# Performance work log

Measured on AMD Instinct MI355X. Metric: run time of the kernel, lower is better.

Reference implementation:

```python
import jax, jax.numpy as jnp
import numpy as np

S, H, I, E, TOP_K = 8192, 2048, 2048, 8, 2


def setup_inputs() -> dict:
    key = jax.random.key(0)
    k0, k1, k2, k3 = jax.random.split(key, 4)
    scale = 1.0 / np.sqrt(H)
    return {
        "hidden_states": jax.random.normal(k0, (S, H), dtype=jnp.float32),
        "w_gate": jax.random.normal(k1, (E, H), dtype=jnp.float32) * scale,
        "w1": jax.random.normal(k2, (E, 2 * I, H), dtype=jnp.float32) * scale,
        "w2": jax.random.normal(k3, (E, H, I), dtype=jnp.float32) * (1.0 / np.sqrt(I)),
        "top_k": TOP_K,
    }


def reference(hidden_states, w_gate, w1, w2, top_k):
    # Router: logits -> float32 softmax -> top-k -> renormalize
    router_logits = hidden_states @ w_gate.T                      # [S, E]
    probs = jax.nn.softmax(router_logits.astype(jnp.float32), axis=-1)
    top_p, top_i = jax.lax.top_k(probs, top_k)                    # [S, k]
    top_p = top_p / jnp.sum(top_p, axis=-1, keepdims=True)

    n_tok, n_exp = probs.shape
    # Dense combine weights [S, E]; zero for non-selected experts.
    combine = jnp.zeros((n_tok, n_exp), dtype=probs.dtype)
    combine = combine.at[jnp.arange(n_tok)[:, None], top_i].add(top_p)

    inter = w2.shape[2]
    out = jnp.zeros_like(hidden_states)
    # Loop over the small fixed expert set; masked-combine gives exact
    # fused_moe semantics (scatter-combine of weighted expert outputs).
    for e in range(n_exp):
        gu = hidden_states @ w1[e].T                              # [S, 2I]
        gate, up = gu[:, :inter], gu[:, inter:]
        h = jax.nn.silu(gate) * up                                # SiluAndMul
        out = out + combine[:, e:e + 1].astype(hidden_states.dtype) * (h @ w2[e].T)
    return out, router_logits
```

## Files before the change

kernel.cpp:

```cpp
#include <hip/hip_runtime.h>
#include <hip/hip_bf16.h>
#include <stdint.h>

#define S_TOK 8192
#define H_DIM 2048
#define I_DIM 2048
#define E_NUM 8

typedef __attribute__((ext_vector_type(4))) float f32x4;
typedef __attribute__((ext_vector_type(8))) short bf16x8;
typedef __attribute__((ext_vector_type(8))) unsigned short u16x8;

#define MFMA16(a, b, c) __builtin_amdgcn_mfma_f32_16x16x32_bf16((a), (b), (c), 0, 0, 0)

__device__ __forceinline__ unsigned short f2bf(float f) {
    unsigned int u = __float_as_uint(f);
    unsigned int r = (u + 0x7FFFu + ((u >> 16) & 1u)) >> 16;
    return (unsigned short)r;
}
__device__ __forceinline__ float bf2f(unsigned short u) {
    return __uint_as_float((unsigned int)u << 16);
}

__device__ __forceinline__ void cvt8(const float* __restrict__ s, unsigned short* __restrict__ d) {
    float4 v0 = *(const float4*)s;
    float4 v1 = *(const float4*)(s + 4);
    u16x8 o;
    o[0] = f2bf(v0.x); o[1] = f2bf(v0.y); o[2] = f2bf(v0.z); o[3] = f2bf(v0.w);
    o[4] = f2bf(v1.x); o[5] = f2bf(v1.y); o[6] = f2bf(v1.z); o[7] = f2bf(v1.w);
    *(u16x8*)d = o;
}

__device__ __forceinline__ void async_copy16(void* lds, const void* g) {
    __builtin_amdgcn_global_load_lds(
        (const __attribute__((address_space(1))) void*)(uintptr_t)g,
        (__attribute__((address_space(3))) void*)(uintptr_t)lds,
        16, 0, 0);
}

__device__ __forceinline__ int xcd_swizzle(int bid, int nwg) {
    int cpx = nwg >> 3;
    return (bid & 7) * cpx + (bid >> 3);
}

__global__ void cvt_kernel(const float* __restrict__ src, unsigned short* __restrict__ dst, long n) {
    long i0 = ((long)blockIdx.x * blockDim.x + threadIdx.x) * 8;
    long stride = (long)gridDim.x * blockDim.x * 8;
    for (long i = i0; i < n; i += stride) cvt8(src + i, dst + i);
}

template<int HALF>
__device__ __forceinline__ void cvt_w1_half_body(const float* __restrict__ src,
                                                 unsigned short* __restrict__ dst,
                                                 long i0, long stride) {
    const long CH = 1L << 21;
    const long TOT = (long)E_NUM * 2 * CH;
    for (long j = i0; j < TOT; j += stride) {
        long e = j >> 22;
        long piece = (j >> 21) & 1;
        long off = j & (CH - 1);
        long g = (e << 23) + ((piece * 2 + HALF) << 21) + off;
        cvt8(src + g, dst + g);
    }
}

__global__ void router_kernel(const float* __restrict__ hs, const float* __restrict__ wg,
                              float* __restrict__ logits,
                              unsigned int* __restrict__ tchoice, float* __restrict__ twgt,
                              unsigned short* __restrict__ hsb,
                              const float* __restrict__ w1src, unsigned short* __restrict__ w1dst,
                              int cvt_blks) {
    if ((int)blockIdx.x >= S_TOK) {
        long i0 = ((long)((int)blockIdx.x - S_TOK) * blockDim.x + threadIdx.x) * 8;
        long stride = (long)cvt_blks * blockDim.x * 8;
        cvt_w1_half_body<0>(w1src, w1dst, i0, stride);
        return;
    }
    int t = blockIdx.x;
    int tid = threadIdx.x;
    const float* hrow = hs + (size_t)t * H_DIM;
    float4 h0 = *(const float4*)(hrow + tid * 8);
    float4 h1 = *(const float4*)(hrow + tid * 8 + 4);
    u16x8 o;
    o[0] = f2bf(h0.x); o[1] = f2bf(h0.y); o[2] = f2bf(h0.z); o[3] = f2bf(h0.w);
    o[4] = f2bf(h1.x); o[5] = f2bf(h1.y); o[6] = f2bf(h1.z); o[7] = f2bf(h1.w);
    *(u16x8*)(hsb + (size_t)t * H_DIM + tid * 8) = o;

    float p[E_NUM];
#pragma unroll
    for (int e = 0; e < E_NUM; ++e) {
        const float* w = wg + (size_t)e * H_DIM + tid * 8;
        float4 w0 = *(const float4*)(w);
        float4 w1v = *(const float4*)(w + 4);
        p[e] = h0.x * w0.x + h0.y * w0.y + h0.z * w0.z + h0.w * w0.w +
               h1.x * w1v.x + h1.y * w1v.y + h1.z * w1v.z + h1.w * w1v.w;
    }
#pragma unroll
    for (int e = 0; e < E_NUM; ++e)
#pragma unroll
        for (int d = 32; d > 0; d >>= 1) p[e] += __shfl_xor(p[e], d, 64);

    __shared__ float red[4][E_NUM];
    int wave = tid >> 6, lane = tid & 63;
    if (lane == 0) {
#pragma unroll
        for (int e = 0; e < E_NUM; ++e) red[wave][e] = p[e];
    }
    __syncthreads();
    if (tid == 0) {
        float l[E_NUM];
#pragma unroll
        for (int e = 0; e < E_NUM; ++e) l[e] = red[0][e] + red[1][e] + red[2][e] + red[3][e];
#pragma unroll
        for (int e = 0; e < E_NUM; ++e) logits[(size_t)t * E_NUM + e] = l[e];
        int i1 = 0;
#pragma unroll
        for (int e = 1; e < E_NUM; ++e) if (l[e] > l[i1]) i1 = e;
        int i2 = (i1 == 0) ? 1 : 0;
#pragma unroll
        for (int e = 0; e < E_NUM; ++e) if (e != i1 && l[e] > l[i2]) i2 = e;
        float b = __expf(l[i2] - l[i1]);
        tchoice[t] = (unsigned)i1 | ((unsigned)i2 << 4);
        twgt[t] = 1.0f / (1.0f + b);
    }
}

__global__ __launch_bounds__(1024) void scan_kernel(
    const unsigned int* __restrict__ tchoice, const float* __restrict__ twgt,
    int* __restrict__ cnt, int* __restrict__ off,
    int* __restrict__ tok_of, float* __restrict__ wgt_of,
    unsigned int* __restrict__ slot_of) {
    __shared__ int lcnt[E_NUM][1024];
    __shared__ int tot[E_NUM];
    int tid = threadIdx.x;
    unsigned int ch[8];
    int c[E_NUM];
#pragma unroll
    for (int e = 0; e < E_NUM; ++e) c[e] = 0;
#pragma unroll
    for (int k = 0; k < 8; ++k) {
        ch[k] = tchoice[tid * 8 + k];
        c[ch[k] & 15]++;
        c[(ch[k] >> 4) & 15]++;
    }
#pragma unroll
    for (int e = 0; e < E_NUM; ++e) lcnt[e][tid] = c[e];
    __syncthreads();
    int wave = tid >> 6, lane = tid & 63;
    if (wave < E_NUM) {
        int base = 0;
        for (int chk = 0; chk < 16; ++chk) {
            int v = lcnt[wave][chk * 64 + lane];
            int inc = v;
#pragma unroll
            for (int d = 1; d < 64; d <<= 1) {
                int u = __shfl_up(inc, d, 64);
                if (lane >= d) inc += u;
            }
            lcnt[wave][chk * 64 + lane] = base + inc - v;
            base += __shfl(inc, 63, 64);
        }
        if (lane == 0) tot[wave] = base;
    }
    __syncthreads();
    if (tid == 0) {
        int s = 0;
#pragma unroll
        for (int e = 0; e < E_NUM; ++e) { off[e] = s; cnt[e] = tot[e]; s += tot[e]; }
    }
    __syncthreads();
#pragma unroll
    for (int e = 0; e < E_NUM; ++e) c[e] = lcnt[e][tid];
#pragma unroll
    for (int k = 0; k < 8; ++k) {
        int t = tid * 8 + k;
        int i1 = ch[k] & 15, i2 = (ch[k] >> 4) & 15;
        float wA = twgt[t];
        int s1 = c[i1]++;
        int s2 = c[i2]++;
        tok_of[i1 * S_TOK + s1] = t; wgt_of[i1 * S_TOK + s1] = wA;
        tok_of[i2 * S_TOK + s2] = t; wgt_of[i2 * S_TOK + s2] = 1.0f - wA;
        slot_of[2 * t]     = ((unsigned)i1 << 20) | (unsigned)s1;
        slot_of[2 * t + 1] = ((unsigned)i2 << 20) | (unsigned)s2;
    }
}

__global__ void combine_kernel(const unsigned short* __restrict__ pbuf,
                               const unsigned int* __restrict__ slot_of,
                               const int* __restrict__ off, float* __restrict__ out) {
    int t = blockIdx.x, tid = threadIdx.x;
    unsigned int a = slot_of[2 * t], b = slot_of[2 * t + 1];
    size_t ra = (size_t)(off[a >> 20] + (int)(a & 0xFFFFFu));
    size_t rb = (size_t)(off[b >> 20] + (int)(b & 0xFFFFFu));
    const unsigned short* pa = pbuf + ra * H_DIM + tid * 8;
    const unsigned short* pb = pbuf + rb * H_DIM + tid * 8;
    ushort4 a0 = *(const ushort4*)pa, a1 = *(const ushort4*)(pa + 4);
    ushort4 b0 = *(const ushort4*)pb, b1 = *(const ushort4*)(pb + 4);
    float4 r0, r1;
    r0.x = bf2f(a0.x) + bf2f(b0.x); r0.y = bf2f(a0.y) + bf2f(b0.y);
    r0.z = bf2f(a0.z) + bf2f(b0.z); r0.w = bf2f(a0.w) + bf2f(b0.w);
    r1.x = bf2f(a1.x) + bf2f(b1.x); r1.y = bf2f(a1.y) + bf2f(b1.y);
    r1.z = bf2f(a1.z) + bf2f(b1.z); r1.w = bf2f(a1.w) + bf2f(b1.w);
    float* op = out + (size_t)t * H_DIM + tid * 8;
    *(float4*)op = r0;
    *(float4*)(op + 4) = r1;
}

template<int IS_G1>
__global__ __launch_bounds__(512, 2) void moe_gemm_kernel(
    const unsigned short* __restrict__ A_src, const unsigned short* __restrict__ W,
    const int* __restrict__ cnt, const int* __restrict__ off,
    const int* __restrict__ tok_of, const float* __restrict__ wgt_of,
    unsigned short* __restrict__ dst,
    const float* __restrict__ cvt_src, unsigned short* __restrict__ cvt_dst,
    long cvt_n, int nt_base, int cvt_mode) {
    const int GRID = E_NUM * 32 * 8;
    int bx = xcd_swizzle(blockIdx.x, GRID);
    int nt_rel = bx / (E_NUM * 32);
    int rr = bx % (E_NUM * 32);
    int e = rr / 32;
    int mt = rr % 32;
    int nt = nt_base + nt_rel;
    int C = cnt[e];
    int live = (C + 255) >> 8;
    int tid = threadIdx.x;

    if (mt >= live) {
        if (cvt_mode == 0) return;
        int S = 0, pre = 0;
#pragma unroll
        for (int ee = 0; ee < E_NUM; ++ee) {
            int nulls = 32 - ((cnt[ee] + 255) >> 8);
            if (ee < e) pre += nulls;
            S += nulls;
        }
        long nrank = (long)nt_rel * S + pre + (mt - live);
        long i0 = (nrank * 512 + tid) * 8;
        long stride = (long)8 * S * 512 * 8;
        if (cvt_mode == 2) {
            cvt_w1_half_body<1>(cvt_src, cvt_dst, i0, stride);
        } else {
            for (long i = i0; i < cvt_n; i += stride) cvt8(cvt_src + i, cvt_dst + i);
        }
        return;
    }
    int O = off[e];

    __shared__ __align__(16) char ldsA[2][32768];
    __shared__ __align__(16) char ldsB[2][32768];

    int wave = tid >> 6, lane = tid & 63;
    int wr = wave >> 2, wc = wave & 3;

    const char* aptr[4];
#pragma unroll
    for (int q = 0; q < 4; ++q) {
        int row = q * 64 + wave * 8 + (lane >> 3);
        int cu = (lane & 7) ^ (row & 7);
        int grow = mt * 256 + row; if (grow > C - 1) grow = C - 1;
        size_t arow = IS_G1 ? (size_t)tok_of[e * S_TOK + grow] : (size_t)(O + grow);
        aptr[q] = (const char*)(A_src + arow * 2048 + cu * 8);
    }
    const char* bptr[4];
#pragma unroll
    for (int j = 0; j < 4; ++j) {
        int lrow = j * 64 + wave * 8 + (lane >> 3);
        int cu = (lane & 7) ^ (lrow & 7);
        int np = lrow >> 7, wcg = (lrow >> 5) & 3, rem = lrow & 31;
        int tbrow = wcg * 64 + np * 32 + rem;
        size_t brow;
        if (IS_G1) {
            int jj = tbrow & 63, wq = tbrow >> 6;
            if (jj < 32) brow = (size_t)(nt * 128 + wq * 32 + jj);
            else         brow = (size_t)I_DIM + nt * 128 + wq * 32 + (jj - 32);
            brow += (size_t)e * (2 * I_DIM);
        } else {
            brow = (size_t)e * H_DIM + nt * 256 + tbrow;
        }
        bptr[j] = (const char*)(W + brow * 2048 + cu * 8);
    }

    int aoff[8][2], boff[4][2];
#pragma unroll
    for (int m = 0; m < 8; ++m)
#pragma unroll
        for (int ks = 0; ks < 2; ++ks) {
            int row = wr * 128 + m * 16 + (lane & 15);
            int cu = ks * 4 + (lane >> 4);
            aoff[m][ks] = row * 128 + ((cu ^ (row & 7)) * 16);
        }
#pragma unroll
    for (int n = 0; n < 4; ++n)
#pragma unroll
        for (int ks = 0; ks < 2; ++ks) {
            int lrow = (n >> 1) * 128 + wc * 32 + (n & 1) * 16 + (lane & 15);
            int cu = ks * 4 + (lane >> 4);
            boff[n][ks] = lrow * 128 + ((cu ^ (lrow & 7)) * 16);
        }

    f32x4 acc[8][4];
#pragma unroll
    for (int m = 0; m < 8; ++m)
#pragma unroll
        for (int n = 0; n < 4; ++n)
#pragma unroll
            for (int q = 0; q < 4; ++q) acc[m][n][q] = 0.0f;

    auto gA = [&](int q, int T, int buf) {
        async_copy16(ldsA[buf] + q * 8192 + wave * 1024, aptr[q] + T * 128);
    };
    auto gB = [&](int j, int T, int buf) {
        async_copy16(ldsB[buf] + j * 8192 + wave * 1024, bptr[j] + T * 128);
    };

    gA(0, 0, 0); gA(2, 0, 0); gA(1, 0, 0); gA(3, 0, 0);
    gB(0, 0, 0); gB(1, 0, 0);
    gA(0, 1, 1); gA(2, 1, 1); gA(1, 1, 1); gA(3, 1, 1);
    gB(2, 0, 0); gB(3, 0, 0);
    asm volatile("s_waitcnt vmcnt(6)" ::: "memory");
    __builtin_amdgcn_s_barrier();

    bf16x8 ar[8][2], br[2][2];
    int cur = 0;
#pragma unroll 2
    for (int T = 0; T < 32; ++T) {
        int nxt = cur ^ 1;
        int TA = (T + 2 < 32) ? T + 2 : 31;
        int TB = (T + 1 < 32) ? T + 1 : 31;
#pragma unroll
        for (int n = 0; n < 2; ++n)
#pragma unroll
            for (int ks = 0; ks < 2; ++ks)
                br[n][ks] = *(const bf16x8*)(ldsB[cur] + boff[n][ks]);
#pragma unroll
        for (int m = 0; m < 4; ++m)
#pragma unroll
            for (int ks = 0; ks < 2; ++ks)
                ar[m][ks] = *(const bf16x8*)(ldsA[cur] + aoff[m][ks]);
        gB(0, TB, nxt); gB(1, TB, nxt);
        __builtin_amdgcn_s_setprio(1);
#pragma unroll
        for (int m = 0; m < 4; ++m)
#pragma unroll
            for (int n = 0; n < 2; ++n) {
                acc[m][n] = MFMA16(ar[m][0], br[n][0], acc[m][n]);
                acc[m][n] = MFMA16(ar[m][1], br[n][1], acc[m][n]);
            }
        __builtin_amdgcn_s_setprio(0);
        __builtin_amdgcn_s_barrier();
#pragma unroll
        for (int m = 4; m < 8; ++m)
#pragma unroll
            for (int ks = 0; ks < 2; ++ks)
                ar[m][ks] = *(const bf16x8*)(ldsA[cur] + aoff[m][ks]);
        gA(0, TA, cur); gA(2, TA, cur);
        __builtin_amdgcn_s_setprio(1);
#pragma unroll
        for (int m = 4; m < 8; ++m)
#pragma unroll
            for (int n = 0; n < 2; ++n) {
                acc[m][n] = MFMA16(ar[m][0], br[n][0], acc[m][n]);
                acc[m][n] = MFMA16(ar[m][1], br[n][1], acc[m][n]);
            }
        __builtin_amdgcn_s_setprio(0);
        asm volatile("s_waitcnt vmcnt(4)" ::: "memory");
        __builtin_amdgcn_s_barrier();
#pragma unroll
        for (int n = 0; n < 2; ++n)
#pragma unroll
            for (int ks = 0; ks < 2; ++ks)
                br[n][ks] = *(const bf16x8*)(ldsB[cur] + boff[n + 2][ks]);
        gA(1, TA, cur); gA(3, TA, cur);
        __builtin_amdgcn_s_setprio(1);
#pragma unroll
        for (int m = 0; m < 4; ++m)
#pragma unroll
            for (int n = 0; n < 2; ++n) {
                acc[m][n + 2] = MFMA16(ar[m][0], br[n][0], acc[m][n + 2]);
                acc[m][n + 2] = MFMA16(ar[m][1], br[n][1], acc[m][n + 2]);
            }
        __builtin_amdgcn_s_setprio(0);
        __builtin_amdgcn_s_barrier();
        gB(2, TB, nxt); gB(3, TB, nxt);
        __builtin_amdgcn_s_setprio(1);
#pragma unroll
        for (int m = 4; m < 8; ++m)
#pragma unroll
            for (int n = 0; n < 2; ++n) {
                acc[m][n + 2] = MFMA16(ar[m][0], br[n][0], acc[m][n + 2]);
                acc[m][n + 2] = MFMA16(ar[m][1], br[n][1], acc[m][n + 2]);
            }
        __builtin_amdgcn_s_setprio(0);
        asm volatile("s_waitcnt vmcnt(6)" ::: "memory");
        __builtin_amdgcn_s_barrier();
        cur = nxt;
    }

    if (IS_G1) {
#pragma unroll
        for (int m = 0; m < 8; ++m)
#pragma unroll
            for (int q = 0; q < 4; ++q) {
                int row = mt * 256 + wr * 128 + m * 16 + (lane >> 4) * 4 + q;
                if (row < C) {
                    float wgt = wgt_of[e * S_TOK + row];
                    unsigned short* hp = dst + (size_t)(O + row) * I_DIM +
                                         nt * 128 + wc * 32 + (lane & 15);
#pragma unroll
                    for (int n = 0; n < 2; ++n) {
                        float g = acc[m][n][q];
                        float u = acc[m][n + 2][q];
                        float hv = (g / (1.0f + __expf(-g))) * u * wgt;
                        hp[n * 16] = f2bf(hv);
                    }
                }
            }
    } else {
#pragma unroll
        for (int m = 0; m < 8; ++m)
#pragma unroll
            for (int q = 0; q < 4; ++q) {
                int row = mt * 256 + wr * 128 + m * 16 + (lane >> 4) * 4 + q;
                if (row < C) {
                    unsigned short* pp = dst + (size_t)(O + row) * H_DIM +
                                         nt * 256 + wc * 64 + (lane & 15);
#pragma unroll
                    for (int n = 0; n < 4; ++n)
                        pp[n * 16] = f2bf(acc[m][n][q]);
                }
            }
    }
}

extern "C" void kernel_launch(void* const* d_in, const int* in_sizes, int n_in,
                              void* d_out, int out_size, void* d_ws, size_t ws_size,
                              hipStream_t stream) {
    const float* hs = (const float*)d_in[0];
    const float* wg = (const float*)d_in[1];
    const float* w1 = (const float*)d_in[2];
    const float* w2 = (const float*)d_in[3];

    float* out = (float*)d_out;
    float* logits = out + (size_t)S_TOK * H_DIM;

    char* ws = (char*)d_ws;
    int* cnt = (int*)ws;
    int* off = (int*)(ws + 256);
    int* tok_of = (int*)(ws + 512);
    float* wgt_of = (float*)(ws + 512 + (size_t)E_NUM * S_TOK * 4);
    unsigned int* slot_of = (unsigned int*)(ws + 512 + (size_t)E_NUM * S_TOK * 8);
    unsigned int* tchoice = (unsigned int*)(ws + 512 + (size_t)E_NUM * S_TOK * 8 + (size_t)S_TOK * 8);
    float* twgt = (float*)(ws + 512 + (size_t)E_NUM * S_TOK * 8 + (size_t)S_TOK * 12);
    size_t o = 512 + (size_t)E_NUM * S_TOK * 8 + (size_t)S_TOK * 16;
    o = (o + 4095) & ~(size_t)4095;
    unsigned short* hsb = (unsigned short*)(ws + o);  o += (size_t)S_TOK * H_DIM * 2;
    unsigned short* wxb = (unsigned short*)(ws + o);  o += (size_t)E_NUM * 2 * I_DIM * H_DIM * 2;
    unsigned short* hbuf = (unsigned short*)(ws + o); o += (size_t)S_TOK * 2 * I_DIM * 2;
    size_t o_w2 = o;
    size_t need_fused = o_w2 + (size_t)E_NUM * H_DIM * I_DIM * 2;
    bool fused = (ws_size >= need_fused);

    const long W1_N = (long)E_NUM * 2 * I_DIM * H_DIM;
    const long W2_N = (long)E_NUM * H_DIM * I_DIM;
    const int GRID = E_NUM * 32 * 8;
    const int CVT_BLKS = 1024;

    if (fused) {
        unsigned short* w2b = (unsigned short*)(ws + o_w2);
        unsigned short* pbuf = wxb;
        router_kernel<<<S_TOK + CVT_BLKS, 256, 0, stream>>>(
            hs, wg, logits, tchoice, twgt, hsb, w1, wxb, CVT_BLKS);
        scan_kernel<<<1, 1024, 0, stream>>>(tchoice, twgt, cnt, off, tok_of, wgt_of, slot_of);
        moe_gemm_kernel<1><<<GRID, 512, 0, stream>>>(
            hsb, wxb, cnt, off, tok_of, wgt_of, hbuf, w1, wxb, 0, 0, 2);
        moe_gemm_kernel<1><<<GRID, 512, 0, stream>>>(
            hsb, wxb, cnt, off, tok_of, wgt_of, hbuf, w2, w2b, W2_N, 8, 1);
        moe_gemm_kernel<0><<<GRID, 512, 0, stream>>>(
            hbuf, w2b, cnt, off, tok_of, wgt_of, pbuf, nullptr, nullptr, 0, 0, 0);
        combine_kernel<<<S_TOK, 256, 0, stream>>>(pbuf, slot_of, off, out);
    } else {
        unsigned short* w2b = wxb;
        unsigned short* pbuf = wxb + (size_t)E_NUM * H_DIM * I_DIM;
        router_kernel<<<S_TOK, 256, 0, stream>>>(
            hs, wg, logits, tchoice, twgt, hsb, nullptr, nullptr, 1);
        scan_kernel<<<1, 1024, 0, stream>>>(tchoice, twgt, cnt, off, tok_of, wgt_of, slot_of);
        cvt_kernel<<<4096, 256, 0, stream>>>(w1, wxb, W1_N);
        moe_gemm_kernel<1><<<GRID, 512, 0, stream>>>(
            hsb, wxb, cnt, off, tok_of, wgt_of, hbuf, nullptr, nullptr, 0, 0, 0);
        moe_gemm_kernel<1><<<GRID, 512, 0, stream>>>(
            hsb, wxb, cnt, off, tok_of, wgt_of, hbuf, nullptr, nullptr, 0, 8, 0);
        cvt_kernel<<<4096, 256, 0, stream>>>(w2, w2b, W2_N);
        moe_gemm_kernel<0><<<GRID, 512, 0, stream>>>(
            hbuf, w2b, cnt, off, tok_of, wgt_of, pbuf, nullptr, nullptr, 0, 0, 0);
        combine_kernel<<<S_TOK, 256, 0, stream>>>(pbuf, slot_of, off, out);
    }
}
```

Baseline: 622.6 us.

## Move weight conversion to dedicated appended blocks and restructure GEMM main loop

```diff
diff --git a/kernel.cpp b/kernel.cpp
--- a/kernel.cpp
+++ b/kernel.cpp
@@ -213,42 +213,30 @@
     const int* __restrict__ tok_of, const float* __restrict__ wgt_of,
     unsigned short* __restrict__ dst,
     const float* __restrict__ cvt_src, unsigned short* __restrict__ cvt_dst,
-    long cvt_n, int nt_base, int cvt_mode) {
-    const int GRID = E_NUM * 32 * 8;
-    int bx = xcd_swizzle(blockIdx.x, GRID);
-    int nt_rel = bx / (E_NUM * 32);
+    long cvt_n, int gemm_grid, int cvt_blks, int nt_base, int cvt_mode) {
+    if ((int)blockIdx.x >= gemm_grid) {
+        long i0 = ((long)((int)blockIdx.x - gemm_grid) * blockDim.x + threadIdx.x) * 8;
+        long stride = (long)cvt_blks * blockDim.x * 8;
+        if (cvt_mode == 2) {
+            cvt_w1_half_body<1>(cvt_src, cvt_dst, i0, stride);
+        } else if (cvt_mode == 1) {
+            for (long i = i0; i < cvt_n; i += stride) cvt8(cvt_src + i, cvt_dst + i);
+        }
+        return;
+    }
+    int bx = xcd_swizzle(blockIdx.x, gemm_grid);
+    int nt = nt_base + bx / (E_NUM * 32);
     int rr = bx % (E_NUM * 32);
     int e = rr / 32;
     int mt = rr % 32;
-    int nt = nt_base + nt_rel;
     int C = cnt[e];
-    int live = (C + 255) >> 8;
-    int tid = threadIdx.x;
-
-    if (mt >= live) {
-        if (cvt_mode == 0) return;
-        int S = 0, pre = 0;
-#pragma unroll
-        for (int ee = 0; ee < E_NUM; ++ee) {
-            int nulls = 32 - ((cnt[ee] + 255) >> 8);
-            if (ee < e) pre += nulls;
-            S += nulls;
-        }
-        long nrank = (long)nt_rel * S + pre + (mt - live);
-        long i0 = (nrank * 512 + tid) * 8;
-        long stride = (long)8 * S * 512 * 8;
-        if (cvt_mode == 2) {
-            cvt_w1_half_body<1>(cvt_src, cvt_dst, i0, stride);
-        } else {
-            for (long i = i0; i < cvt_n; i += stride) cvt8(cvt_src + i, cvt_dst + i);
-        }
-        return;
-    }
+    if (mt * 256 >= C) return;
     int O = off[e];
 
     __shared__ __align__(16) char ldsA[2][32768];
     __shared__ __align__(16) char ldsB[2][32768];
 
+    int tid = threadIdx.x;
     int wave = tid >> 6, lane = tid & 63;
     int wr = wave >> 2, wc = wave & 3;
 
@@ -313,14 +301,13 @@
         async_copy16(ldsB[buf] + j * 8192 + wave * 1024, bptr[j] + T * 128);
     };
 
-    gA(0, 0, 0); gA(2, 0, 0); gA(1, 0, 0); gA(3, 0, 0);
-    gB(0, 0, 0); gB(1, 0, 0);
-    gA(0, 1, 1); gA(2, 1, 1); gA(1, 1, 1); gA(3, 1, 1);
-    gB(2, 0, 0); gB(3, 0, 0);
-    asm volatile("s_waitcnt vmcnt(6)" ::: "memory");
+    gA(0, 0, 0); gA(1, 0, 0); gA(2, 0, 0); gA(3, 0, 0);
+    gB(0, 0, 0); gB(1, 0, 0); gB(2, 0, 0); gB(3, 0, 0);
+    gA(0, 1, 1); gA(1, 1, 1); gA(2, 1, 1); gA(3, 1, 1);
+    asm volatile("s_waitcnt vmcnt(4)" ::: "memory");
     __builtin_amdgcn_s_barrier();
 
-    bf16x8 ar[8][2], br[2][2];
+    bf16x8 ar[8][2], br[4][2];
     int cur = 0;
 #pragma unroll 2
     for (int T = 0; T < 32; ++T) {
@@ -333,11 +320,16 @@
             for (int ks = 0; ks < 2; ++ks)
                 br[n][ks] = *(const bf16x8*)(ldsB[cur] + boff[n][ks]);
 #pragma unroll
-        for (int m = 0; m < 4; ++m)
+        for (int m = 0; m < 8; ++m)
 #pragma unroll
             for (int ks = 0; ks < 2; ++ks)
                 ar[m][ks] = *(const bf16x8*)(ldsA[cur] + aoff[m][ks]);
-        gB(0, TB, nxt); gB(1, TB, nxt);
+#pragma unroll
+        for (int n = 2; n < 4; ++n)
+#pragma unroll
+            for (int ks = 0; ks < 2; ++ks)
+                br[n][ks] = *(const bf16x8*)(ldsB[cur] + boff[n][ks]);
+        gB(0, TB, nxt); gB(1, TB, nxt); gB(2, TB, nxt); gB(3, TB, nxt);
         __builtin_amdgcn_s_setprio(1);
 #pragma unroll
         for (int m = 0; m < 4; ++m)
@@ -348,11 +340,6 @@
             }
         __builtin_amdgcn_s_setprio(0);
         __builtin_amdgcn_s_barrier();
-#pragma unroll
-        for (int m = 4; m < 8; ++m)
-#pragma unroll
-            for (int ks = 0; ks < 2; ++ks)
-                ar[m][ks] = *(const bf16x8*)(ldsA[cur] + aoff[m][ks]);
         gA(0, TA, cur); gA(2, TA, cur);
         __builtin_amdgcn_s_setprio(1);
 #pragma unroll
@@ -363,35 +350,18 @@
                 acc[m][n] = MFMA16(ar[m][1], br[n][1], acc[m][n]);
             }
         __builtin_amdgcn_s_setprio(0);
-        asm volatile("s_waitcnt vmcnt(4)" ::: "memory");
         __builtin_amdgcn_s_barrier();
-#pragma unroll
-        for (int n = 0; n < 2; ++n)
-#pragma unroll
-            for (int ks = 0; ks < 2; ++ks)
-                br[n][ks] = *(const bf16x8*)(ldsB[cur] + boff[n + 2][ks]);
         gA(1, TA, cur); gA(3, TA, cur);
         __builtin_amdgcn_s_setprio(1);
 #pragma unroll
-        for (int m = 0; m < 4; ++m)
+        for (int m = 0; m < 8; ++m)
 #pragma unroll
             for (int n = 0; n < 2; ++n) {
-                acc[m][n + 2] = MFMA16(ar[m][0], br[n][0], acc[m][n + 2]);
-                acc[m][n + 2] = MFMA16(ar[m][1], br[n][1], acc[m][n + 2]);
+                acc[m][n + 2] = MFMA16(ar[m][0], br[n + 2][0], acc[m][n + 2]);
+                acc[m][n + 2] = MFMA16(ar[m][1], br[n + 2][1], acc[m][n + 2]);
             }
         __builtin_amdgcn_s_setprio(0);
-        __builtin_amdgcn_s_barrier();
-        gB(2, TB, nxt); gB(3, TB, nxt);
-        __builtin_amdgcn_s_setprio(1);
-#pragma unroll
-        for (int m = 4; m < 8; ++m)
-#pragma unroll
-            for (int n = 0; n < 2; ++n) {
-                acc[m][n + 2] = MFMA16(ar[m][0], br[n][0], acc[m][n + 2]);
-                acc[m][n + 2] = MFMA16(ar[m][1], br[n][1], acc[m][n + 2]);
-            }
-        __builtin_amdgcn_s_setprio(0);
-        asm volatile("s_waitcnt vmcnt(6)" ::: "memory");
+        asm volatile("s_waitcnt vmcnt(4)" ::: "memory");
         __builtin_amdgcn_s_barrier();
         cur = nxt;
     }
@@ -471,12 +441,15 @@
         router_kernel<<<S_TOK + CVT_BLKS, 256, 0, stream>>>(
             hs, wg, logits, tchoice, twgt, hsb, w1, wxb, CVT_BLKS);
         scan_kernel<<<1, 1024, 0, stream>>>(tchoice, twgt, cnt, off, tok_of, wgt_of, slot_of);
-        moe_gemm_kernel<1><<<GRID, 512, 0, stream>>>(
-            hsb, wxb, cnt, off, tok_of, wgt_of, hbuf, w1, wxb, 0, 0, 2);
-        moe_gemm_kernel<1><<<GRID, 512, 0, stream>>>(
-            hsb, wxb, cnt, off, tok_of, wgt_of, hbuf, w2, w2b, W2_N, 8, 1);
+        moe_gemm_kernel<1><<<GRID + CVT_BLKS, 512, 0, stream>>>(
+            hsb, wxb, cnt, off, tok_of, wgt_of, hbuf,
+            w1, wxb, 0, GRID, CVT_BLKS, 0, 2);
+        moe_gemm_kernel<1><<<GRID + CVT_BLKS, 512, 0, stream>>>(
+            hsb, wxb, cnt, off, tok_of, wgt_of, hbuf,
+            w2, w2b, W2_N, GRID, CVT_BLKS, 8, 1);
         moe_gemm_kernel<0><<<GRID, 512, 0, stream>>>(
-            hbuf, w2b, cnt, off, tok_of, wgt_of, pbuf, nullptr, nullptr, 0, 0, 0);
+            hbuf, w2b, cnt, off, tok_of, wgt_of, pbuf,
+            nullptr, nullptr, 0, GRID, 0, 0, 0);
         combine_kernel<<<S_TOK, 256, 0, stream>>>(pbuf, slot_of, off, out);
     } else {
         unsigned short* w2b = wxb;
@@ -486,12 +459,12 @@
         scan_kernel<<<1, 1024, 0, stream>>>(tchoice, twgt, cnt, off, tok_of, wgt_of, slot_of);
         cvt_kernel<<<4096, 256, 0, stream>>>(w1, wxb, W1_N);
         moe_gemm_kernel<1><<<GRID, 512, 0, stream>>>(
-            hsb, wxb, cnt, off, tok_of, wgt_of, hbuf, nullptr, nullptr, 0, 0, 0);
+            hsb, wxb, cnt, off, tok_of, wgt_of, hbuf, nullptr, nullptr, 0, GRID, 0, 0, 0);
         moe_gemm_kernel<1><<<GRID, 512, 0, stream>>>(
-            hsb, wxb, cnt, off, tok_of, wgt_of, hbuf, nullptr, nullptr, 0, 8, 0);
+            hsb, wxb, cnt, off, tok_of, wgt_of, hbuf, nullptr, nullptr, 0, GRID, 0, 8, 0);
         cvt_kernel<<<4096, 256, 0, stream>>>(w2, w2b, W2_N);
         moe_gemm_kernel<0><<<GRID, 512, 0, stream>>>(
-            hbuf, w2b, cnt, off, tok_of, wgt_of, pbuf, nullptr, nullptr, 0, 0, 0);
+            hbuf, w2b, cnt, off, tok_of, wgt_of, pbuf, nullptr, nullptr, 0, GRID, 0, 0, 0);
         combine_kernel<<<S_TOK, 256, 0, stream>>>(pbuf, slot_of, off, out);
     }
 }
```

Result: no change. 616.2 us (-1.0%).
